# Kernel optimization log

Hardware: AMD Instinct MI355X
Metric: run time of the kernel (lower is better)

The kernel has to match this reference:

```python
import jax, jax.numpy as jnp
import numpy as np

N, E = 50000, 800000
IN, H = 128, 128
NTYPE, NSCHOOL, NTIME, NAUTHOR = 20, 30, 15, 200


def setup_inputs() -> dict:
    key = jax.random.key(0)
    ks = jax.random.split(key, 20)

    def lin(k, i, o):  # kaiming-ish init
        return jax.random.normal(k, (i, o), jnp.float32) * (1.0 / np.sqrt(i))

    return {
        "x0": jax.random.normal(ks[0], (N, IN), jnp.float32),
        "edge_index": jax.random.randint(ks[1], (2, E), 0, N, dtype=jnp.int64),
        # GCNConv weights (x @ W + b after aggregation)
        "W1": lin(ks[2], IN, H),   "b1": jnp.zeros((H,), jnp.float32),
        "Wt": lin(ks[3], H, NTYPE),    "bt": jnp.zeros((NTYPE,), jnp.float32),
        "Ws": lin(ks[4], H, NSCHOOL), "bs": jnp.zeros((NSCHOOL,), jnp.float32),
        "Wa": lin(ks[5], H, NAUTHOR), "ba": jnp.zeros((NAUTHOR,), jnp.float32),
        # classification heads (Linear stored as [in, out])
        "Wct": lin(ks[6], NTYPE, NTYPE),       "bct": jnp.zeros((NTYPE,), jnp.float32),
        "Wcs": lin(ks[7], NSCHOOL, NSCHOOL), "bcs": jnp.zeros((NSCHOOL,), jnp.float32),
        "Wtf": lin(ks[8], IN, NTIME),          "btf": jnp.zeros((NTIME,), jnp.float32),
        "Wca": lin(ks[9], NAUTHOR, NAUTHOR), "bca": jnp.zeros((NAUTHOR,), jnp.float32),
    }


def reference(x0, edge_index, W1, b1, Wt, bt, Ws, bs, Wa, ba,
              Wct, bct, Wcs, bcs, Wtf, btf, Wca, bca):
    n = x0.shape[0]
    src, dst = edge_index[0], edge_index[1]
    # GCNConv default: add self-loops, symmetric deg^{-1/2} normalization
    loop = jnp.arange(n, dtype=edge_index.dtype)
    src_f = jnp.concatenate([src, loop])  # [E+N]
    dst_f = jnp.concatenate([dst, loop])
    deg = jax.ops.segment_sum(jnp.ones(src_f.shape[0], jnp.float32), dst_f, num_segments=n)
    dinv = jnp.where(deg > 0, jax.lax.rsqrt(deg), 0.0)
    norm = dinv[src_f] * dinv[dst_f]  # [E+N]

    def conv(x, W, b):
        xt = x @ W                                   # transform first (small out dim)
        msg = xt[src_f] * norm[:, None]              # [E+N, out]
        return jax.ops.segment_sum(msg, dst_f, num_segments=n) + b

    h = jax.nn.relu(conv(x0, W1, b1))  # dropout is identity at inference

    out_type = jax.nn.softmax(conv(h, Wt, bt) @ Wct + bct, axis=-1)
    out_school = jax.nn.softmax(conv(h, Ws, bs) @ Wcs + bcs, axis=-1)
    out_time = jax.nn.softmax(x0 @ Wtf + btf, axis=-1)  # head reads x0 directly
    out_author = jax.nn.softmax(conv(h, Wa, ba) @ Wca + bca, axis=-1)
    return (out_type, out_school, out_time, out_author)
```

## Files before the change

kernel.cpp:

```cpp
#include <hip/hip_runtime.h>
#include <math.h>


typedef short short8 __attribute__((ext_vector_type(8)));
typedef float f32x4 __attribute__((ext_vector_type(4)));

static __device__ __forceinline__ unsigned short f2bf(float x) {
  unsigned u = __float_as_uint(x);
  u += 0x7fff + ((u >> 16) & 1);
  return (unsigned short)(u >> 16);
}
static __device__ __forceinline__ unsigned pack2bf(float lo, float hi) {
  return ((unsigned)f2bf(hi) << 16) | (unsigned)f2bf(lo);
}
static __device__ __forceinline__ float bflo(unsigned u) {
  return __uint_as_float(u << 16);
}
static __device__ __forceinline__ float bfhi(unsigned u) {
  return __uint_as_float(u & 0xffff0000u);
}

__global__ void k_deg(const int* __restrict__ dst, int E, int* __restrict__ deg) {
  int e = blockIdx.x * blockDim.x + threadIdx.x;
  if (e < E) atomicAdd(&deg[dst[e]], 1);
}

__global__ void k_scan1(const int* __restrict__ deg, int n,
                        int* __restrict__ excl, int* __restrict__ bsum) {
  __shared__ int sm[256];
  int i = blockIdx.x * 256 + threadIdx.x;
  int v = (i < n) ? deg[i] : 0;
  sm[threadIdx.x] = v;
  __syncthreads();
#pragma unroll
  for (int o = 1; o < 256; o <<= 1) {
    int t = (threadIdx.x >= o) ? sm[threadIdx.x - o] : 0;
    __syncthreads();
    sm[threadIdx.x] += t;
    __syncthreads();
  }
  if (i < n) excl[i] = sm[threadIdx.x] - v;
  if (threadIdx.x == 255) bsum[blockIdx.x] = sm[255];
}

__global__ void k_scan2(int* __restrict__ bsum, int nb) {
  __shared__ int sm[256];
  int v = (threadIdx.x < nb) ? bsum[threadIdx.x] : 0;
  sm[threadIdx.x] = v;
  __syncthreads();
#pragma unroll
  for (int o = 1; o < 256; o <<= 1) {
    int t = (threadIdx.x >= o) ? sm[threadIdx.x - o] : 0;
    __syncthreads();
    sm[threadIdx.x] += t;
    __syncthreads();
  }
  if (threadIdx.x < nb) bsum[threadIdx.x] = sm[threadIdx.x] - v;
}

__global__ void k_finalize(int* __restrict__ row_off, const int* __restrict__ bsum,
                           const int* __restrict__ deg, int* __restrict__ cursor,
                           float* __restrict__ dinv, int n) {
  int i = blockIdx.x * 256 + threadIdx.x;
  if (i < n) {
    int ro = row_off[i] + bsum[blockIdx.x];
    row_off[i] = ro;
    cursor[i] = ro;
    dinv[i] = rsqrtf((float)(deg[i] + 1));
  }
}

__global__ void k_fill(const int* __restrict__ src, const int* __restrict__ dst,
                       int E, int* __restrict__ cursor,
                       unsigned short* __restrict__ csr) {
  int e = blockIdx.x * blockDim.x + threadIdx.x;
  if (e < E) {
    int d = dst[e];
    int p = atomicAdd(&cursor[d], 1);
    csr[p] = (unsigned short)src[e];
  }
}

__global__ __launch_bounds__(256) void k_scale(
    const float* __restrict__ X, const float* __restrict__ dinv,
    unsigned* __restrict__ Y, int n) {
  int t = blockIdx.x * 256 + threadIdx.x;
  int total = n * 64;
  if (t < total) {
    int row = t >> 6;
    float d = dinv[row];
    float2 v = reinterpret_cast<const float2*>(X)[t];
    Y[t] = pack2bf(v.x * d, v.y * d);
  }
}

__global__ __launch_bounds__(256) void k_agg(
    const unsigned* __restrict__ Y, unsigned* __restrict__ out,
    const int* __restrict__ row_off, const int* __restrict__ deg,
    const unsigned short* __restrict__ csr, const float* __restrict__ dinv,
    int n) {
  int wave = threadIdx.x >> 6;
  int lane = threadIdx.x & 63;
  int sub = lane >> 5;
  int sl = lane & 31;
  int i = blockIdx.x * 8 + wave * 2 + sub;
  if (i >= n) return;
  int start = row_off[i];
  int cnt = deg[i];
  const uint2* Yv = reinterpret_cast<const uint2*>(Y);
  float a0 = 0.f, a1 = 0.f, a2 = 0.f, a3 = 0.f;
  int j = 0;
  for (; j + 3 < cnt; j += 4) {
    int s0 = csr[start + j];
    int s1 = csr[start + j + 1];
    int s2 = csr[start + j + 2];
    int s3 = csr[start + j + 3];
    uint2 u0 = Yv[(size_t)s0 * 32 + sl];
    uint2 u1 = Yv[(size_t)s1 * 32 + sl];
    uint2 u2 = Yv[(size_t)s2 * 32 + sl];
    uint2 u3 = Yv[(size_t)s3 * 32 + sl];
    a0 += (bflo(u0.x) + bflo(u1.x)) + (bflo(u2.x) + bflo(u3.x));
    a1 += (bfhi(u0.x) + bfhi(u1.x)) + (bfhi(u2.x) + bfhi(u3.x));
    a2 += (bflo(u0.y) + bflo(u1.y)) + (bflo(u2.y) + bflo(u3.y));
    a3 += (bfhi(u0.y) + bfhi(u1.y)) + (bfhi(u2.y) + bfhi(u3.y));
  }
  for (; j < cnt; ++j) {
    int s0 = csr[start + j];
    uint2 u0 = Yv[(size_t)s0 * 32 + sl];
    a0 += bflo(u0.x);
    a1 += bfhi(u0.x);
    a2 += bflo(u0.y);
    a3 += bfhi(u0.y);
  }
  uint2 us = Yv[(size_t)i * 32 + sl];
  float di = dinv[i];
  uint2 r;
  r.x = pack2bf((a0 + bflo(us.x)) * di, (a1 + bfhi(us.x)) * di);
  r.y = pack2bf((a2 + bflo(us.y)) * di, (a3 + bfhi(us.y)) * di);
  reinterpret_cast<uint2*>(out)[(size_t)i * 32 + sl] = r;
}

__global__ void k_pack128(const float* __restrict__ W, unsigned short* __restrict__ P) {
  int t = blockIdx.x * 256 + threadIdx.x;
  int i = t >> 7, c = t & 127;
  P[((i >> 3) * 128 + c) * 8 + (i & 7)] = f2bf(W[t]);
}

__global__ void k_fuse(const float* __restrict__ Wt, const float* __restrict__ bt,
                       const float* __restrict__ Wct, const float* __restrict__ bct,
                       const float* __restrict__ Ws, const float* __restrict__ bs,
                       const float* __restrict__ Wcs, const float* __restrict__ bcs,
                       const float* __restrict__ Wa, const float* __restrict__ ba,
                       const float* __restrict__ Wca, const float* __restrict__ bca,
                       unsigned short* __restrict__ WfPk, float* __restrict__ bf) {
  int c = blockIdx.x;
  int i = threadIdx.x;
  float acc = 0.f, bacc = 0.f;
  if (c < 20) {
    for (int k = 0; k < 20; ++k) {
      float w2 = Wct[k * 20 + c];
      acc += Wt[i * 20 + k] * w2;
      bacc += bt[k] * w2;
    }
    bacc += bct[c];
  } else if (c < 50) {
    int cc = c - 20;
    for (int k = 0; k < 30; ++k) {
      float w2 = Wcs[k * 30 + cc];
      acc += Ws[i * 30 + k] * w2;
      bacc += bs[k] * w2;
    }
    bacc += bcs[cc];
  } else if (c < 250) {
    int cc = c - 50;
    for (int k = 0; k < 200; ++k) {
      float w2 = Wca[k * 200 + cc];
      acc += Wa[i * 200 + k] * w2;
      bacc += ba[k] * w2;
    }
    bacc += bca[cc];
  }
  WfPk[((i >> 3) * 256 + c) * 8 + (i & 7)] = f2bf(acc);
  if (i == 0) bf[c] = bacc;
}

static __device__ __forceinline__ void stage32(
    const short* __restrict__ A, short (*sAb)[136], int rowBase, int n, int tid) {
  for (int t = tid; t < 32 * 16; t += 256) {
    int r = t >> 4, c8 = t & 15;
    int gr = rowBase + r;
    short8 v = (short8){0, 0, 0, 0, 0, 0, 0, 0};
    if (gr < n) v = *reinterpret_cast<const short8*>(A + (size_t)gr * 128 + c8 * 8);
    *reinterpret_cast<short8*>(&sAb[r][c8 * 8]) = v;
  }
}

__global__ __launch_bounds__(256) void k_mfma_gemm128(
    const short* __restrict__ A, const unsigned short* __restrict__ Wpk,
    const float* __restrict__ bias, const float* __restrict__ dinv,
    unsigned short* __restrict__ out, int n) {
  __shared__ short sAb[32][136];
  int rowBase = blockIdx.x * 32;
  stage32(A, sAb, rowBase, n, threadIdx.x);
  __syncthreads();
  int wave = threadIdx.x >> 6, lane = threadIdx.x & 63;
  int rg = wave >> 1, ch = wave & 1;
  int lr = lane & 15, lg = lane >> 4;
  int r0 = rowBase + rg * 16;
  short8 afr[4];
#pragma unroll
  for (int kk = 0; kk < 4; ++kk)
    afr[kk] = *reinterpret_cast<const short8*>(&sAb[rg * 16 + lr][kk * 32 + lg * 8]);
  f32x4 acc[4];
#pragma unroll
  for (int t = 0; t < 4; ++t) acc[t] = (f32x4){0.f, 0.f, 0.f, 0.f};
  const short8* Wp8 = reinterpret_cast<const short8*>(Wpk);
#pragma unroll
  for (int t = 0; t < 4; ++t) {
#pragma unroll
    for (int kk = 0; kk < 4; ++kk) {
      short8 bfr = Wp8[(kk * 4 + lg) * 128 + ch * 64 + t * 16 + lr];
      acc[t] = __builtin_amdgcn_mfma_f32_16x16x32_bf16(afr[kk], bfr, acc[t], 0, 0, 0);
    }
  }
  int rloc = r0 + lg * 4;
#pragma unroll
  for (int t = 0; t < 4; ++t) {
    int col = ch * 64 + t * 16 + lr;
    float b = bias[col];
#pragma unroll
    for (int reg = 0; reg < 4; ++reg) {
      int row = rloc + reg;
      if (row < n) {
        float v = fmaxf(acc[t][reg] + b, 0.f) * dinv[row];
        out[(size_t)row * 128 + col] = f2bf(v);
      }
    }
  }
}

__global__ __launch_bounds__(256) void k_heads_fused(
    const short* __restrict__ A, const unsigned short* __restrict__ Wpk,
    const float* __restrict__ bf, float* __restrict__ outT,
    float* __restrict__ outS, float* __restrict__ outA, int n) {
  __shared__ short sAb[32][136];
  __shared__ float aM[2][2][16];
  __shared__ float aS[2][2][16];
  int rowBase = blockIdx.x * 32;
  stage32(A, sAb, rowBase, n, threadIdx.x);
  __syncthreads();
  int wave = threadIdx.x >> 6, lane = threadIdx.x & 63;
  int rg = wave >> 1, ch = wave & 1;
  int lr = lane & 15, lg = lane >> 4;
  int r0 = rowBase + rg * 16;
  int cb = ch * 128;
  short8 afr[4];
#pragma unroll
  for (int kk = 0; kk < 4; ++kk)
    afr[kk] = *reinterpret_cast<const short8*>(&sAb[rg * 16 + lr][kk * 32 + lg * 8]);
  f32x4 acc[8];
#pragma unroll
  for (int t = 0; t < 8; ++t) acc[t] = (f32x4){0.f, 0.f, 0.f, 0.f};
  const short8* Wp8 = reinterpret_cast<const short8*>(Wpk);
#pragma unroll
  for (int t = 0; t < 8; ++t) {
#pragma unroll
    for (int kk = 0; kk < 4; ++kk) {
      short8 bfr = Wp8[(kk * 4 + lg) * 256 + cb + t * 16 + lr];
      acc[t] = __builtin_amdgcn_mfma_f32_16x16x32_bf16(afr[kk], bfr, acc[t], 0, 0, 0);
    }
  }
  float bias_l[8];
#pragma unroll
  for (int t = 0; t < 8; ++t) bias_l[t] = bf[cb + t * 16 + lr];
  float mTr[4], mSr[4], mAr[4];
#pragma unroll
  for (int reg = 0; reg < 4; ++reg) {
    float mT = -INFINITY, mS = -INFINITY, mA = -INFINITY;
#pragma unroll
    for (int t = 0; t < 8; ++t) {
      int c = cb + t * 16 + lr;
      float val = acc[t][reg] + bias_l[t];
      acc[t][reg] = val;
      if (c < 20) mT = fmaxf(mT, val);
      else if (c < 50) mS = fmaxf(mS, val);
      else if (c < 250) mA = fmaxf(mA, val);
    }
#pragma unroll
    for (int o = 8; o; o >>= 1) {
      mT = fmaxf(mT, __shfl_xor(mT, o, 64));
      mS = fmaxf(mS, __shfl_xor(mS, o, 64));
      mA = fmaxf(mA, __shfl_xor(mA, o, 64));
    }
    mTr[reg] = mT; mSr[reg] = mS; mAr[reg] = mA;
    if (lr == 0) aM[rg][ch][lg * 4 + reg] = mA;
  }
  __syncthreads();
#pragma unroll
  for (int reg = 0; reg < 4; ++reg)
    mAr[reg] = fmaxf(mAr[reg], aM[rg][ch ^ 1][lg * 4 + reg]);
  float sTr[4], sSr[4], sAr[4];
#pragma unroll
  for (int reg = 0; reg < 4; ++reg) {
    float sT = 0.f, sS = 0.f, sA = 0.f;
#pragma unroll
    for (int t = 0; t < 8; ++t) {
      int c = cb + t * 16 + lr;
      float m = (c < 20) ? mTr[reg] : (c < 50) ? mSr[reg] : mAr[reg];
      float e = __expf(acc[t][reg] - m);
      acc[t][reg] = e;
      if (c < 20) sT += e;
      else if (c < 50) sS += e;
      else if (c < 250) sA += e;
    }
#pragma unroll
    for (int o = 8; o; o >>= 1) {
      sT += __shfl_xor(sT, o, 64);
      sS += __shfl_xor(sS, o, 64);
      sA += __shfl_xor(sA, o, 64);
    }
    sTr[reg] = sT; sSr[reg] = sS; sAr[reg] = sA;
    if (lr == 0) aS[rg][ch][lg * 4 + reg] = sA;
  }
  __syncthreads();
#pragma unroll
  for (int reg = 0; reg < 4; ++reg)
    sAr[reg] += aS[rg][ch ^ 1][lg * 4 + reg];
  int rloc = r0 + lg * 4;
#pragma unroll
  for (int reg = 0; reg < 4; ++reg) {
    int row = rloc + reg;
    if (row >= n) continue;
    float iT = 1.f / sTr[reg], iS = 1.f / sSr[reg], iA = 1.f / sAr[reg];
#pragma unroll
    for (int t = 0; t < 8; ++t) {
      int c = cb + t * 16 + lr;
      float e = acc[t][reg];
      if (c < 20) outT[(size_t)row * 20 + c] = e * iT;
      else if (c < 50) outS[(size_t)row * 30 + (c - 20)] = e * iS;
      else if (c < 250) outA[(size_t)row * 200 + (c - 50)] = e * iA;
    }
  }
}

__global__ __launch_bounds__(256) void k_time(
    const float* __restrict__ x0, const float* __restrict__ Wtf,
    const float* __restrict__ btf, float* __restrict__ outT, int n) {
  __shared__ float sW[128][16];
  __shared__ float sb[16];
  for (int t = threadIdx.x; t < 128 * 16; t += 256) {
    int k = t >> 4, j = t & 15;
    sW[k][j] = (j < 15) ? Wtf[k * 15 + j] : 0.f;
  }
  if (threadIdx.x < 16) sb[threadIdx.x] = (threadIdx.x < 15) ? btf[threadIdx.x] : 0.f;
  __syncthreads();
  int j = threadIdx.x & 15;
  int rl = threadIdx.x >> 4;
  int r = blockIdx.x * 16 + rl;
  if (r >= n) return;
  float acc = sb[j];
  const float4* xr = reinterpret_cast<const float4*>(x0 + (size_t)r * 128);
  for (int k4 = 0; k4 < 32; ++k4) {
    float4 xv = xr[k4];
    acc += xv.x * sW[k4 * 4 + 0][j] + xv.y * sW[k4 * 4 + 1][j] +
           xv.z * sW[k4 * 4 + 2][j] + xv.w * sW[k4 * 4 + 3][j];
  }
  float m = (j < 15) ? acc : -INFINITY;
#pragma unroll
  for (int o = 8; o; o >>= 1) m = fmaxf(m, __shfl_xor(m, o, 16));
  float e = (j < 15) ? __expf(acc - m) : 0.f;
  float s = e;
#pragma unroll
  for (int o = 8; o; o >>= 1) s += __shfl_xor(s, o, 16);
  if (j < 15) outT[(size_t)r * 15 + j] = e / s;
}

extern "C" void kernel_launch(void* const* d_in, const int* in_sizes, int n_in,
                              void* d_out, int out_size, void* d_ws, size_t ws_size,
                              hipStream_t stream) {
  const float* x0 = (const float*)d_in[0];
  const int* ei = (const int*)d_in[1];
  const float* W1 = (const float*)d_in[2];
  const float* b1 = (const float*)d_in[3];
  const float* Wt = (const float*)d_in[4];
  const float* bt = (const float*)d_in[5];
  const float* Ws = (const float*)d_in[6];
  const float* bs = (const float*)d_in[7];
  const float* Wa = (const float*)d_in[8];
  const float* ba = (const float*)d_in[9];
  const float* Wct = (const float*)d_in[10];
  const float* bct = (const float*)d_in[11];
  const float* Wcs = (const float*)d_in[12];
  const float* bcs = (const float*)d_in[13];
  const float* Wtf = (const float*)d_in[14];
  const float* btf = (const float*)d_in[15];
  const float* Wca = (const float*)d_in[16];
  const float* bca = (const float*)d_in[17];
  (void)n_in; (void)out_size; (void)ws_size;

  int N = in_sizes[0] / 128;
  int E = in_sizes[1] / 2;
  float* out = (float*)d_out;

  char* ws = (char*)d_ws;
  size_t off = 0;
  auto alloc = [&](size_t bytes) -> void* {
    void* p = ws + off;
    off = (off + bytes + 255) & ~(size_t)255;
    return p;
  };
  int* deg = (int*)alloc((size_t)N * 4);
  int* row_off = (int*)alloc((size_t)N * 4);
  int* bsum = (int*)alloc(256 * 4);
  int* cursor = (int*)alloc((size_t)N * 4);
  float* dinv = (float*)alloc((size_t)N * 4);
  unsigned short* csr = (unsigned short*)alloc((size_t)E * 2);
  unsigned short* WfPk = (unsigned short*)alloc((size_t)128 * 256 * 2);
  unsigned short* W1Pk = (unsigned short*)alloc((size_t)128 * 128 * 2);
  float* bf = (float*)alloc(256 * 4);
  unsigned* Yb = (unsigned*)alloc((size_t)N * 64 * 4);
  unsigned* Ab = (unsigned*)alloc((size_t)N * 64 * 4);
  unsigned* Bb = (unsigned*)alloc((size_t)N * 64 * 4);

  const int* srcp = ei;
  const int* dstp = ei + E;
  int gE = (E + 255) / 256;
  int gN = (N + 255) / 256;
  int g32 = (N + 31) / 32;

  hipMemsetAsync(deg, 0, (size_t)N * 4, stream);
  k_deg<<<gE, 256, 0, stream>>>(dstp, E, deg);
  k_scan1<<<gN, 256, 0, stream>>>(deg, N, row_off, bsum);
  k_scan2<<<1, 256, 0, stream>>>(bsum, gN);
  k_finalize<<<gN, 256, 0, stream>>>(row_off, bsum, deg, cursor, dinv, N);
  k_fill<<<gE, 256, 0, stream>>>(srcp, dstp, E, cursor, csr);
  k_pack128<<<64, 256, 0, stream>>>(W1, W1Pk);
  k_fuse<<<256, 128, 0, stream>>>(Wt, bt, Wct, bct, Ws, bs, Wcs, bcs, Wa, ba, Wca,
                                  bca, WfPk, bf);
  k_scale<<<(N * 64 + 255) / 256, 256, 0, stream>>>(x0, dinv, Yb, N);
  k_agg<<<(N + 7) / 8, 256, 0, stream>>>(Yb, Ab, row_off, deg, csr, dinv, N);
  k_mfma_gemm128<<<g32, 256, 0, stream>>>(
      (const short*)Ab, W1Pk, b1, dinv, (unsigned short*)Bb, N);
  k_agg<<<(N + 7) / 8, 256, 0, stream>>>(Bb, Ab, row_off, deg, csr, dinv, N);
  k_heads_fused<<<g32, 256, 0, stream>>>(
      (const short*)Ab, WfPk, bf, out, out + (size_t)N * 20, out + (size_t)N * 65, N);
  k_time<<<(N + 15) / 16, 256, 0, stream>>>(x0, Wtf, btf, out + (size_t)N * 50, N);
}
```

Before: 340.2 us.

## Range-partition degree and CSR fill atomics; fuse finalize+scale and weight packing

Degree counting and CSR fill now run with each block scanning a chunk of edges but only handling destinations in one of 8 node ranges. Since blockIdx&7 selects the range, the 8 blocks sharing a chunk run close together and their atomics land in disjoint regions, which should improve L2 locality across XCDs. Finalize is merged into the scale kernel, and W1 packing is folded into the head-weight fusion kernel, cutting the launch count. In exchange, every edge's dst is read 8 times, and the fused scale kernel recomputes rsqrt per element.

```diff
diff --git a/kernel.cpp b/kernel.cpp
--- a/kernel.cpp
+++ b/kernel.cpp
@@ -4,6 +4,8 @@
 
 typedef short short8 __attribute__((ext_vector_type(8)));
 typedef float f32x4 __attribute__((ext_vector_type(4)));
+
+#define FILL_CHUNK 2048
 
 static __device__ __forceinline__ unsigned short f2bf(float x) {
   unsigned u = __float_as_uint(x);
@@ -20,9 +22,18 @@
   return __uint_as_float(u & 0xffff0000u);
 }
 
-__global__ void k_deg(const int* __restrict__ dst, int E, int* __restrict__ deg) {
-  int e = blockIdx.x * blockDim.x + threadIdx.x;
-  if (e < E) atomicAdd(&deg[dst[e]], 1);
+__global__ __launch_bounds__(256) void k_deg_x(
+    const int* __restrict__ dst, int E, int* __restrict__ deg, int rlen) {
+  int rng = blockIdx.x & 7;
+  int chunk = blockIdx.x >> 3;
+  int lo = rng * rlen, hi = lo + rlen;
+  int base = chunk * FILL_CHUNK;
+  int end = base + FILL_CHUNK;
+  if (end > E) end = E;
+  for (int e = base + threadIdx.x; e < end; e += 256) {
+    int d = dst[e];
+    if (d >= lo && d < hi) atomicAdd(&deg[d], 1);
+  }
 }
 
 __global__ void k_scan1(const int* __restrict__ deg, int n,
@@ -58,39 +69,40 @@
   if (threadIdx.x < nb) bsum[threadIdx.x] = sm[threadIdx.x] - v;
 }
 
-__global__ void k_finalize(int* __restrict__ row_off, const int* __restrict__ bsum,
-                           const int* __restrict__ deg, int* __restrict__ cursor,
-                           float* __restrict__ dinv, int n) {
-  int i = blockIdx.x * 256 + threadIdx.x;
-  if (i < n) {
-    int ro = row_off[i] + bsum[blockIdx.x];
-    row_off[i] = ro;
-    cursor[i] = ro;
-    dinv[i] = rsqrtf((float)(deg[i] + 1));
-  }
-}
-
-__global__ void k_fill(const int* __restrict__ src, const int* __restrict__ dst,
-                       int E, int* __restrict__ cursor,
-                       unsigned short* __restrict__ csr) {
-  int e = blockIdx.x * blockDim.x + threadIdx.x;
-  if (e < E) {
+__global__ __launch_bounds__(256) void k_finscale(
+    const float* __restrict__ X, const int* __restrict__ deg,
+    const int* __restrict__ bsum, int* __restrict__ row_off,
+    int* __restrict__ cursor, float* __restrict__ dinv,
+    unsigned* __restrict__ Y, int n) {
+  int p = blockIdx.x * 256 + threadIdx.x;
+  if (p >= n * 64) return;
+  int row = p >> 6;
+  float d = rsqrtf((float)(deg[row] + 1));
+  if ((p & 63) == 0) {
+    int ro = row_off[row] + bsum[row >> 8];
+    row_off[row] = ro;
+    cursor[row] = ro;
+    dinv[row] = d;
+  }
+  float2 v = reinterpret_cast<const float2*>(X)[p];
+  Y[p] = pack2bf(v.x * d, v.y * d);
+}
+
+__global__ __launch_bounds__(256) void k_fill_x(
+    const int* __restrict__ src, const int* __restrict__ dst, int E,
+    int* __restrict__ cursor, unsigned short* __restrict__ csr, int rlen) {
+  int rng = blockIdx.x & 7;
+  int chunk = blockIdx.x >> 3;
+  int lo = rng * rlen, hi = lo + rlen;
+  int base = chunk * FILL_CHUNK;
+  int end = base + FILL_CHUNK;
+  if (end > E) end = E;
+  for (int e = base + threadIdx.x; e < end; e += 256) {
     int d = dst[e];
-    int p = atomicAdd(&cursor[d], 1);
-    csr[p] = (unsigned short)src[e];
-  }
-}
-
-__global__ __launch_bounds__(256) void k_scale(
-    const float* __restrict__ X, const float* __restrict__ dinv,
-    unsigned* __restrict__ Y, int n) {
-  int t = blockIdx.x * 256 + threadIdx.x;
-  int total = n * 64;
-  if (t < total) {
-    int row = t >> 6;
-    float d = dinv[row];
-    float2 v = reinterpret_cast<const float2*>(X)[t];
-    Y[t] = pack2bf(v.x * d, v.y * d);
+    if (d >= lo && d < hi) {
+      int p = atomicAdd(&cursor[d], 1);
+      csr[p] = (unsigned short)src[e];
+    }
   }
 }
 
@@ -140,19 +152,21 @@
   reinterpret_cast<uint2*>(out)[(size_t)i * 32 + sl] = r;
 }
 
-__global__ void k_pack128(const float* __restrict__ W, unsigned short* __restrict__ P) {
-  int t = blockIdx.x * 256 + threadIdx.x;
-  int i = t >> 7, c = t & 127;
-  P[((i >> 3) * 128 + c) * 8 + (i & 7)] = f2bf(W[t]);
-}
-
-__global__ void k_fuse(const float* __restrict__ Wt, const float* __restrict__ bt,
-                       const float* __restrict__ Wct, const float* __restrict__ bct,
-                       const float* __restrict__ Ws, const float* __restrict__ bs,
-                       const float* __restrict__ Wcs, const float* __restrict__ bcs,
-                       const float* __restrict__ Wa, const float* __restrict__ ba,
-                       const float* __restrict__ Wca, const float* __restrict__ bca,
-                       unsigned short* __restrict__ WfPk, float* __restrict__ bf) {
+__global__ void k_fusepack(
+    const float* __restrict__ Wt, const float* __restrict__ bt,
+    const float* __restrict__ Wct, const float* __restrict__ bct,
+    const float* __restrict__ Ws, const float* __restrict__ bs,
+    const float* __restrict__ Wcs, const float* __restrict__ bcs,
+    const float* __restrict__ Wa, const float* __restrict__ ba,
+    const float* __restrict__ Wca, const float* __restrict__ bca,
+    unsigned short* __restrict__ WfPk, float* __restrict__ bf,
+    const float* __restrict__ W1, unsigned short* __restrict__ W1Pk) {
+  if (blockIdx.x >= 256) {
+    int t = (blockIdx.x - 256) * 128 + threadIdx.x;
+    int i = t >> 7, c = t & 127;
+    W1Pk[((i >> 3) * 128 + c) * 8 + (i & 7)] = f2bf(W1[t]);
+    return;
+  }
   int c = blockIdx.x;
   int i = threadIdx.x;
   float acc = 0.f, bacc = 0.f;
@@ -424,20 +438,20 @@
 
   const int* srcp = ei;
   const int* dstp = ei + E;
-  int gE = (E + 255) / 256;
   int gN = (N + 255) / 256;
   int g32 = (N + 31) / 32;
+  int rlen = (N + 7) / 8;
+  int gX = 8 * ((E + FILL_CHUNK - 1) / FILL_CHUNK);
 
   hipMemsetAsync(deg, 0, (size_t)N * 4, stream);
-  k_deg<<<gE, 256, 0, stream>>>(dstp, E, deg);
+  k_deg_x<<<gX, 256, 0, stream>>>(dstp, E, deg, rlen);
   k_scan1<<<gN, 256, 0, stream>>>(deg, N, row_off, bsum);
   k_scan2<<<1, 256, 0, stream>>>(bsum, gN);
-  k_finalize<<<gN, 256, 0, stream>>>(row_off, bsum, deg, cursor, dinv, N);
-  k_fill<<<gE, 256, 0, stream>>>(srcp, dstp, E, cursor, csr);
-  k_pack128<<<64, 256, 0, stream>>>(W1, W1Pk);
-  k_fuse<<<256, 128, 0, stream>>>(Wt, bt, Wct, bct, Ws, bs, Wcs, bcs, Wa, ba, Wca,
-                                  bca, WfPk, bf);
-  k_scale<<<(N * 64 + 255) / 256, 256, 0, stream>>>(x0, dinv, Yb, N);
+  k_finscale<<<(N * 64 + 255) / 256, 256, 0, stream>>>(
+      x0, deg, bsum, row_off, cursor, dinv, Yb, N);
+  k_fill_x<<<gX, 256, 0, stream>>>(srcp, dstp, E, cursor, csr, rlen);
+  k_fusepack<<<384, 128, 0, stream>>>(Wt, bt, Wct, bct, Ws, bs, Wcs, bcs, Wa, ba,
+                                      Wca, bca, WfPk, bf, W1, W1Pk);
   k_agg<<<(N + 7) / 8, 256, 0, stream>>>(Yb, Ab, row_off, deg, csr, dinv, N);
   k_mfma_gemm128<<<g32, 256, 0, stream>>>(
       (const short*)Ab, W1Pk, b1, dinv, (unsigned short*)Bb, N);
```

Result: no change. 336.8 us (-1.0%).

## Merge graph setup phases into one cooperative kernel and fuse time head

Applied to the files above, without the earlier changes.

Replaces the memset, degree, two scan, finalize, fill, weight-pack, head-fusion and scale kernels with a single cooperative kernel that runs those phases separated by grid-wide syncs. The time-head softmax is folded into the heads kernel as extra blocks, and it now reads Wtf from global memory instead of staging it in shared memory. The aim is to remove many launch gaps and small-kernel tails. The cost is grid.sync overhead, and the grid is capped at 256*occ blocks, so the atomic-heavy phases run with fewer blocks.

```diff
diff --git a/kernel.cpp b/kernel.cpp
--- a/kernel.cpp
+++ b/kernel.cpp
@@ -1,6 +1,9 @@
 #include <hip/hip_runtime.h>
+#include <hip/hip_cooperative_groups.h>
 #include <math.h>
 
+
+namespace cg = cooperative_groups;
 
 typedef short short8 __attribute__((ext_vector_type(8)));
 typedef float f32x4 __attribute__((ext_vector_type(4)));
@@ -20,78 +23,154 @@
   return __uint_as_float(u & 0xffff0000u);
 }
 
-__global__ void k_deg(const int* __restrict__ dst, int E, int* __restrict__ deg) {
-  int e = blockIdx.x * blockDim.x + threadIdx.x;
-  if (e < E) atomicAdd(&deg[dst[e]], 1);
-}
-
-__global__ void k_scan1(const int* __restrict__ deg, int n,
-                        int* __restrict__ excl, int* __restrict__ bsum) {
-  __shared__ int sm[256];
-  int i = blockIdx.x * 256 + threadIdx.x;
-  int v = (i < n) ? deg[i] : 0;
-  sm[threadIdx.x] = v;
+struct GP {
+  const float* x0;
+  const int* src;
+  const int* dst;
+  const float* W1;
+  const float *Wt, *bt, *Wct, *bct;
+  const float *Ws, *bs, *Wcs, *bcs;
+  const float *Wa, *ba, *Wca, *bca;
+  int* deg;
+  int* row_off;
+  int* bsum;
+  int* cursor;
+  float* dinv;
+  unsigned short* csr;
+  unsigned short* WfPk;
+  unsigned short* W1Pk;
+  float* bfb;
+  unsigned* Yb;
+  int N, E, gN;
+};
+
+static __device__ __forceinline__ void ph_zero_fuse(const GP& p, int bid, int nb,
+                                                    int tid) {
+  for (int i = bid * 256 + tid; i < p.N; i += nb * 256) p.deg[i] = 0;
+  for (int w = bid; w < 384; w += nb) {
+    int i = tid;
+    if (i < 128) {
+      if (w >= 256) {
+        int t = (w - 256) * 128 + i;
+        int r = t >> 7, c = t & 127;
+        p.W1Pk[((r >> 3) * 128 + c) * 8 + (r & 7)] = f2bf(p.W1[t]);
+      } else {
+        int c = w;
+        float acc = 0.f, bacc = 0.f;
+        if (c < 20) {
+          for (int k = 0; k < 20; ++k) {
+            float w2 = p.Wct[k * 20 + c];
+            acc += p.Wt[i * 20 + k] * w2;
+            bacc += p.bt[k] * w2;
+          }
+          bacc += p.bct[c];
+        } else if (c < 50) {
+          int cc = c - 20;
+          for (int k = 0; k < 30; ++k) {
+            float w2 = p.Wcs[k * 30 + cc];
+            acc += p.Ws[i * 30 + k] * w2;
+            bacc += p.bs[k] * w2;
+          }
+          bacc += p.bcs[cc];
+        } else if (c < 250) {
+          int cc = c - 50;
+          for (int k = 0; k < 200; ++k) {
+            float w2 = p.Wca[k * 200 + cc];
+            acc += p.Wa[i * 200 + k] * w2;
+            bacc += p.ba[k] * w2;
+          }
+          bacc += p.bca[cc];
+        }
+        p.WfPk[((i >> 3) * 256 + c) * 8 + (i & 7)] = f2bf(acc);
+        if (i == 0) p.bfb[c] = bacc;
+      }
+    }
+  }
+}
+
+static __device__ __forceinline__ void ph_deg(const GP& p, int bid, int nb,
+                                              int tid) {
+  for (int e = bid * 256 + tid; e < p.E; e += nb * 256)
+    atomicAdd(&p.deg[p.dst[e]], 1);
+}
+
+static __device__ __forceinline__ void ph_scan_chunks(const GP& p, int bid,
+                                                      int nb, int tid,
+                                                      int* smi) {
+  for (int c = bid; c < p.gN; c += nb) {
+    int i = c * 256 + tid;
+    int v = (i < p.N) ? p.deg[i] : 0;
+    smi[tid] = v;
+    __syncthreads();
+#pragma unroll
+    for (int o = 1; o < 256; o <<= 1) {
+      int t = (tid >= o) ? smi[tid - o] : 0;
+      __syncthreads();
+      smi[tid] += t;
+      __syncthreads();
+    }
+    if (i < p.N) p.row_off[i] = smi[tid] - v;
+    if (tid == 255) p.bsum[c] = smi[255];
+    __syncthreads();
+  }
+}
+
+static __device__ __forceinline__ void ph_scan_bsum(const GP& p, int tid,
+                                                    int* smi) {
+  int v = (tid < p.gN) ? p.bsum[tid] : 0;
+  smi[tid] = v;
   __syncthreads();
 #pragma unroll
   for (int o = 1; o < 256; o <<= 1) {
-    int t = (threadIdx.x >= o) ? sm[threadIdx.x - o] : 0;
+    int t = (tid >= o) ? smi[tid - o] : 0;
     __syncthreads();
-    sm[threadIdx.x] += t;
+    smi[tid] += t;
     __syncthreads();
   }
-  if (i < n) excl[i] = sm[threadIdx.x] - v;
-  if (threadIdx.x == 255) bsum[blockIdx.x] = sm[255];
-}
-
-__global__ void k_scan2(int* __restrict__ bsum, int nb) {
-  __shared__ int sm[256];
-  int v = (threadIdx.x < nb) ? bsum[threadIdx.x] : 0;
-  sm[threadIdx.x] = v;
-  __syncthreads();
-#pragma unroll
-  for (int o = 1; o < 256; o <<= 1) {
-    int t = (threadIdx.x >= o) ? sm[threadIdx.x - o] : 0;
-    __syncthreads();
-    sm[threadIdx.x] += t;
-    __syncthreads();
-  }
-  if (threadIdx.x < nb) bsum[threadIdx.x] = sm[threadIdx.x] - v;
-}
-
-__global__ void k_finalize(int* __restrict__ row_off, const int* __restrict__ bsum,
-                           const int* __restrict__ deg, int* __restrict__ cursor,
-                           float* __restrict__ dinv, int n) {
-  int i = blockIdx.x * 256 + threadIdx.x;
-  if (i < n) {
-    int ro = row_off[i] + bsum[blockIdx.x];
-    row_off[i] = ro;
-    cursor[i] = ro;
-    dinv[i] = rsqrtf((float)(deg[i] + 1));
-  }
-}
-
-__global__ void k_fill(const int* __restrict__ src, const int* __restrict__ dst,
-                       int E, int* __restrict__ cursor,
-                       unsigned short* __restrict__ csr) {
-  int e = blockIdx.x * blockDim.x + threadIdx.x;
-  if (e < E) {
-    int d = dst[e];
-    int p = atomicAdd(&cursor[d], 1);
-    csr[p] = (unsigned short)src[e];
-  }
-}
-
-__global__ __launch_bounds__(256) void k_scale(
-    const float* __restrict__ X, const float* __restrict__ dinv,
-    unsigned* __restrict__ Y, int n) {
-  int t = blockIdx.x * 256 + threadIdx.x;
-  int total = n * 64;
-  if (t < total) {
-    int row = t >> 6;
-    float d = dinv[row];
-    float2 v = reinterpret_cast<const float2*>(X)[t];
-    Y[t] = pack2bf(v.x * d, v.y * d);
-  }
+  if (tid < p.gN) p.bsum[tid] = smi[tid] - v;
+}
+
+static __device__ __forceinline__ void ph_finscale(const GP& p, int bid, int nb,
+                                                   int tid) {
+  int total = p.N * 64;
+  for (int q = bid * 256 + tid; q < total; q += nb * 256) {
+    int row = q >> 6;
+    float d = rsqrtf((float)(p.deg[row] + 1));
+    if ((q & 63) == 0) {
+      int ro = p.row_off[row] + p.bsum[row >> 8];
+      p.row_off[row] = ro;
+      p.cursor[row] = ro;
+      p.dinv[row] = d;
+    }
+    float2 v = reinterpret_cast<const float2*>(p.x0)[q];
+    p.Yb[q] = pack2bf(v.x * d, v.y * d);
+  }
+}
+
+static __device__ __forceinline__ void ph_fill(const GP& p, int bid, int nb,
+                                               int tid) {
+  for (int e = bid * 256 + tid; e < p.E; e += nb * 256) {
+    int d = p.dst[e];
+    int pos = atomicAdd(&p.cursor[d], 1);
+    p.csr[pos] = (unsigned short)p.src[e];
+  }
+}
+
+__global__ __launch_bounds__(256) void k_setup_coop(GP p) {
+  cg::grid_group grid = cg::this_grid();
+  __shared__ int smi[256];
+  int bid = blockIdx.x, nb = gridDim.x, tid = threadIdx.x;
+  ph_zero_fuse(p, bid, nb, tid);
+  grid.sync();
+  ph_deg(p, bid, nb, tid);
+  grid.sync();
+  ph_scan_chunks(p, bid, nb, tid, smi);
+  grid.sync();
+  if (bid == 0) ph_scan_bsum(p, tid, smi);
+  grid.sync();
+  ph_finscale(p, bid, nb, tid);
+  grid.sync();
+  ph_fill(p, bid, nb, tid);
 }
 
 __global__ __launch_bounds__(256) void k_agg(
@@ -140,50 +219,6 @@
   reinterpret_cast<uint2*>(out)[(size_t)i * 32 + sl] = r;
 }
 
-__global__ void k_pack128(const float* __restrict__ W, unsigned short* __restrict__ P) {
-  int t = blockIdx.x * 256 + threadIdx.x;
-  int i = t >> 7, c = t & 127;
-  P[((i >> 3) * 128 + c) * 8 + (i & 7)] = f2bf(W[t]);
-}
-
-__global__ void k_fuse(const float* __restrict__ Wt, const float* __restrict__ bt,
-                       const float* __restrict__ Wct, const float* __restrict__ bct,
-                       const float* __restrict__ Ws, const float* __restrict__ bs,
-                       const float* __restrict__ Wcs, const float* __restrict__ bcs,
-                       const float* __restrict__ Wa, const float* __restrict__ ba,
-                       const float* __restrict__ Wca, const float* __restrict__ bca,
-                       unsigned short* __restrict__ WfPk, float* __restrict__ bf) {
-  int c = blockIdx.x;
-  int i = threadIdx.x;
-  float acc = 0.f, bacc = 0.f;
-  if (c < 20) {
-    for (int k = 0; k < 20; ++k) {
-      float w2 = Wct[k * 20 + c];
-      acc += Wt[i * 20 + k] * w2;
-      bacc += bt[k] * w2;
-    }
-    bacc += bct[c];
-  } else if (c < 50) {
-    int cc = c - 20;
-    for (int k = 0; k < 30; ++k) {
-      float w2 = Wcs[k * 30 + cc];
-      acc += Ws[i * 30 + k] * w2;
-      bacc += bs[k] * w2;
-    }
-    bacc += bcs[cc];
-  } else if (c < 250) {
-    int cc = c - 50;
-    for (int k = 0; k < 200; ++k) {
-      float w2 = Wca[k * 200 + cc];
-      acc += Wa[i * 200 + k] * w2;
-      bacc += ba[k] * w2;
-    }
-    bacc += bca[cc];
-  }
-  WfPk[((i >> 3) * 256 + c) * 8 + (i & 7)] = f2bf(acc);
-  if (i == 0) bf[c] = bacc;
-}
-
 static __device__ __forceinline__ void stage32(
     const short* __restrict__ A, short (*sAb)[136], int rowBase, int n, int tid) {
   for (int t = tid; t < 32 * 16; t += 256) {
@@ -239,10 +274,37 @@
   }
 }
 
-__global__ __launch_bounds__(256) void k_heads_fused(
+__global__ __launch_bounds__(256) void k_heads_time(
     const short* __restrict__ A, const unsigned short* __restrict__ Wpk,
-    const float* __restrict__ bf, float* __restrict__ outT,
-    float* __restrict__ outS, float* __restrict__ outA, int n) {
+    const float* __restrict__ bfb, const float* __restrict__ x0,
+    const float* __restrict__ Wtf, const float* __restrict__ btf,
+    float* __restrict__ outT, float* __restrict__ outS,
+    float* __restrict__ outTime, float* __restrict__ outA, int n) {
+  int g32 = (n + 31) / 32;
+  if ((int)blockIdx.x >= g32) {
+    int tb = blockIdx.x - g32;
+    int j = threadIdx.x & 15;
+    int rl = threadIdx.x >> 4;
+    int r = tb * 16 + rl;
+    if (r >= n) return;
+    int jj = (j < 15) ? j : 14;
+    float acc = btf[jj];
+    const float4* xr = reinterpret_cast<const float4*>(x0 + (size_t)r * 128);
+    for (int k4 = 0; k4 < 32; ++k4) {
+      float4 xv = xr[k4];
+      acc += xv.x * Wtf[(k4 * 4 + 0) * 15 + jj] + xv.y * Wtf[(k4 * 4 + 1) * 15 + jj] +
+             xv.z * Wtf[(k4 * 4 + 2) * 15 + jj] + xv.w * Wtf[(k4 * 4 + 3) * 15 + jj];
+    }
+    float m = (j < 15) ? acc : -INFINITY;
+#pragma unroll
+    for (int o = 8; o; o >>= 1) m = fmaxf(m, __shfl_xor(m, o, 16));
+    float e = (j < 15) ? __expf(acc - m) : 0.f;
+    float s = e;
+#pragma unroll
+    for (int o = 8; o; o >>= 1) s += __shfl_xor(s, o, 16);
+    if (j < 15) outTime[(size_t)r * 15 + j] = e / s;
+    return;
+  }
   __shared__ short sAb[32][136];
   __shared__ float aM[2][2][16];
   __shared__ float aS[2][2][16];
@@ -272,7 +334,7 @@
   }
   float bias_l[8];
 #pragma unroll
-  for (int t = 0; t < 8; ++t) bias_l[t] = bf[cb + t * 16 + lr];
+  for (int t = 0; t < 8; ++t) bias_l[t] = bfb[cb + t * 16 + lr];
   float mTr[4], mSr[4], mAr[4];
 #pragma unroll
   for (int reg = 0; reg < 4; ++reg) {
@@ -341,38 +403,6 @@
       else if (c < 250) outA[(size_t)row * 200 + (c - 50)] = e * iA;
     }
   }
-}
-
-__global__ __launch_bounds__(256) void k_time(
-    const float* __restrict__ x0, const float* __restrict__ Wtf,
-    const float* __restrict__ btf, float* __restrict__ outT, int n) {
-  __shared__ float sW[128][16];
-  __shared__ float sb[16];
-  for (int t = threadIdx.x; t < 128 * 16; t += 256) {
-    int k = t >> 4, j = t & 15;
-    sW[k][j] = (j < 15) ? Wtf[k * 15 + j] : 0.f;
-  }
-  if (threadIdx.x < 16) sb[threadIdx.x] = (threadIdx.x < 15) ? btf[threadIdx.x] : 0.f;
-  __syncthreads();
-  int j = threadIdx.x & 15;
-  int rl = threadIdx.x >> 4;
-  int r = blockIdx.x * 16 + rl;
-  if (r >= n) return;
-  float acc = sb[j];
-  const float4* xr = reinterpret_cast<const float4*>(x0 + (size_t)r * 128);
-  for (int k4 = 0; k4 < 32; ++k4) {
-    float4 xv = xr[k4];
-    acc += xv.x * sW[k4 * 4 + 0][j] + xv.y * sW[k4 * 4 + 1][j] +
-           xv.z * sW[k4 * 4 + 2][j] + xv.w * sW[k4 * 4 + 3][j];
-  }
-  float m = (j < 15) ? acc : -INFINITY;
-#pragma unroll
-  for (int o = 8; o; o >>= 1) m = fmaxf(m, __shfl_xor(m, o, 16));
-  float e = (j < 15) ? __expf(acc - m) : 0.f;
-  float s = e;
-#pragma unroll
-  for (int o = 8; o; o >>= 1) s += __shfl_xor(s, o, 16);
-  if (j < 15) outT[(size_t)r * 15 + j] = e / s;
 }
 
 extern "C" void kernel_launch(void* const* d_in, const int* in_sizes, int n_in,
@@ -417,32 +447,40 @@
   unsigned short* csr = (unsigned short*)alloc((size_t)E * 2);
   unsigned short* WfPk = (unsigned short*)alloc((size_t)128 * 256 * 2);
   unsigned short* W1Pk = (unsigned short*)alloc((size_t)128 * 128 * 2);
-  float* bf = (float*)alloc(256 * 4);
+  float* bfb = (float*)alloc(256 * 4);
   unsigned* Yb = (unsigned*)alloc((size_t)N * 64 * 4);
   unsigned* Ab = (unsigned*)alloc((size_t)N * 64 * 4);
   unsigned* Bb = (unsigned*)alloc((size_t)N * 64 * 4);
 
-  const int* srcp = ei;
-  const int* dstp = ei + E;
-  int gE = (E + 255) / 256;
-  int gN = (N + 255) / 256;
+  GP gp;
+  gp.x0 = x0;
+  gp.src = ei;
+  gp.dst = ei + E;
+  gp.W1 = W1;
+  gp.Wt = Wt; gp.bt = bt; gp.Wct = Wct; gp.bct = bct;
+  gp.Ws = Ws; gp.bs = bs; gp.Wcs = Wcs; gp.bcs = bcs;
+  gp.Wa = Wa; gp.ba = ba; gp.Wca = Wca; gp.bca = bca;
+  gp.deg = deg; gp.row_off = row_off; gp.bsum = bsum; gp.cursor = cursor;
+  gp.dinv = dinv; gp.csr = csr; gp.WfPk = WfPk; gp.W1Pk = W1Pk; gp.bfb = bfb;
+  gp.Yb = Yb;
+  gp.N = N; gp.E = E; gp.gN = (N + 255) / 256;
+
+  int occ = 0;
+  hipOccupancyMaxActiveBlocksPerMultiprocessor(&occ, k_setup_coop, 256, 0);
+  if (occ < 1) occ = 1;
+  if (occ > 4) occ = 4;
+  int sgrid = 256 * occ;
+  void* kargs[] = {(void*)&gp};
+  hipLaunchCooperativeKernel((void*)k_setup_coop, dim3(sgrid), dim3(256), kargs,
+                             0, stream);
+
   int g32 = (N + 31) / 32;
-
-  hipMemsetAsync(deg, 0, (size_t)N * 4, stream);
-  k_deg<<<gE, 256, 0, stream>>>(dstp, E, deg);
-  k_scan1<<<gN, 256, 0, stream>>>(deg, N, row_off, bsum);
-  k_scan2<<<1, 256, 0, stream>>>(bsum, gN);
-  k_finalize<<<gN, 256, 0, stream>>>(row_off, bsum, deg, cursor, dinv, N);
-  k_fill<<<gE, 256, 0, stream>>>(srcp, dstp, E, cursor, csr);
-  k_pack128<<<64, 256, 0, stream>>>(W1, W1Pk);
-  k_fuse<<<256, 128, 0, stream>>>(Wt, bt, Wct, bct, Ws, bs, Wcs, bcs, Wa, ba, Wca,
-                                  bca, WfPk, bf);
-  k_scale<<<(N * 64 + 255) / 256, 256, 0, stream>>>(x0, dinv, Yb, N);
+  int gT = (N + 15) / 16;
   k_agg<<<(N + 7) / 8, 256, 0, stream>>>(Yb, Ab, row_off, deg, csr, dinv, N);
   k_mfma_gemm128<<<g32, 256, 0, stream>>>(
       (const short*)Ab, W1Pk, b1, dinv, (unsigned short*)Bb, N);
   k_agg<<<(N + 7) / 8, 256, 0, stream>>>(Bb, Ab, row_off, deg, csr, dinv, N);
-  k_heads_fused<<<g32, 256, 0, stream>>>(
-      (const short*)Ab, WfPk, bf, out, out + (size_t)N * 20, out + (size_t)N * 65, N);
-  k_time<<<(N + 15) / 16, 256, 0, stream>>>(x0, Wtf, btf, out + (size_t)N * 50, N);
-}
+  k_heads_time<<<g32 + gT, 256, 0, stream>>>(
+      (const short*)Ab, WfPk, bfb, x0, Wtf, btf,
+      out, out + (size_t)N * 20, out + (size_t)N * 50, out + (size_t)N * 65, N);
+}
```

Result: slower. 529.2 us (+55.6%).
